# Kernel tuning notes

Measured on AMD Instinct MI355X. Metric: run time of the kernel, lower is better.

Reference implementation:

```python
import jax, jax.numpy as jnp
import numpy as np

BATCH, T, IN, HID = 64, 2048, 128, 256

def setup_inputs() -> dict:
    key = jax.random.key(0)
    ks = jax.random.split(key, 6)
    s = 0.05
    return {
        "x": jax.random.normal(ks[0], (BATCH, T, IN), dtype=jnp.float32),
        "w_ih0": jax.random.normal(ks[1], (IN, 4 * HID), dtype=jnp.float32) * s,
        "w_hh0": jax.random.normal(ks[2], (HID, 4 * HID), dtype=jnp.float32) * s,
        "b0": jnp.zeros((4 * HID,), dtype=jnp.float32),
        "w_ih1": jax.random.normal(ks[3], (HID, 4 * HID), dtype=jnp.float32) * s,
        "w_hh1": jax.random.normal(ks[4], (HID, 4 * HID), dtype=jnp.float32) * s,
        "b1": jnp.zeros((4 * HID,), dtype=jnp.float32),
    }

def _run_layer(xs, h0, c0, w_ih, w_hh, b):
    # xs: [T, B, D]. Original code iterates input_[T-1-t], i.e. reversed time.
    def step(carry, xt):
        h, c = carry
        gates = xt @ w_ih + h @ w_hh + b            # [B, 4H]
        f, i, o, g = jnp.split(gates, 4, axis=1)     # split order f,i,o,g as in source
        c1 = jax.nn.sigmoid(f) * c + jax.nn.sigmoid(i) * jnp.tanh(g)
        h1 = jax.nn.sigmoid(o) * jnp.tanh(c1)
        return (h1, c1), h1
    (hT, cT), ys = jax.lax.scan(step, (h0, c0), xs[::-1])
    return ys, hT, cT

def reference(x, w_ih0, w_hh0, b0, w_ih1, w_hh1, b1):
    xs = jnp.transpose(x, (1, 0, 2))                 # batch_first -> [T, B, IN]
    B = xs.shape[1]
    H = w_hh0.shape[0]
    h0 = jnp.zeros((B, H), dtype=xs.dtype)
    # Both layers start from the SAME zero hx (faithful to source).
    y0, hn0, cn0 = _run_layer(xs, h0, h0, w_ih0, w_hh0, b0)
    y1, hn1, cn1 = _run_layer(y0, h0, h0, w_ih1, w_hh1, b1)
    # Source never transposes output back: output is [T, B, H]
    return y1, (jnp.stack([hn0, hn1], 0), jnp.stack([cn0, cn1], 0))
```

## Files before the change

### kernel.cpp

```cpp
#include <hip/hip_runtime.h>
#include <cstdint>
#include <cstddef>

#define T_STEPS 2048
#define NBATCH  64
#define HID     256
#define NGATE   1024
#define NROWS   (T_STEPS*NBATCH)

#define KR   192
#define KRC  24
#define KLC  8
#define REC_LDS_BYTES (KLC*1024*16 + 4096 + 512)

typedef _Float16 f16x8 __attribute__((ext_vector_type(8)));
typedef _Float16 h2f   __attribute__((ext_vector_type(2)));
typedef float    f32x4 __attribute__((ext_vector_type(4)));

__device__ __forceinline__ unsigned short f2h_bits(float f) {
    _Float16 h = (_Float16)f;
    return __builtin_bit_cast(unsigned short, h);
}
__device__ __forceinline__ float h2f_scalar(unsigned short u) {
    return (float)__builtin_bit_cast(_Float16, u);
}
__device__ __forceinline__ h2f bch(unsigned int u) {
    return __builtin_bit_cast(h2f, u);
}

#define OFF_G    ((size_t)0)
#define OFF_Y0   ((size_t)268435456)
#define OFF_WT0  ((size_t)335544320)
#define OFF_WT1  ((size_t)336068608)
#define OFF_LW0  ((size_t)336592896)
#define OFF_LW1  ((size_t)336723968)
#define OFF_BS0  ((size_t)336855040)
#define OFF_BS1  ((size_t)337117184)
#define WS_NEED  ((size_t)337641472)

__global__ void convert_weights(const float* __restrict__ w_ih0, const float* __restrict__ w_hh0,
                                const float* __restrict__ w_ih1, const float* __restrict__ w_hh1,
                                unsigned short* __restrict__ WT0, unsigned short* __restrict__ WT1,
                                unsigned short* __restrict__ LW0, unsigned short* __restrict__ LW1,
                                unsigned short* __restrict__ BS0, unsigned short* __restrict__ BS1)
{
    int gid = blockIdx.x * blockDim.x + threadIdx.x;
    int gsz = gridDim.x * blockDim.x;
    for (int s = gid; s < 1024 * 256; s += gsz) {
        int j = s >> 8, k = s & 255;
        WT0[s] = f2h_bits(w_hh0[k * 1024 + j]);
        WT1[s] = f2h_bits(w_hh1[k * 1024 + j]);
    }
    for (int s = gid; s < KLC * 1024 * 8; s += gsz) {
        int i = s & 7, j = (s >> 3) & 1023, c = s >> 13;
        int k = KR + c * 8 + i;
        LW0[s] = f2h_bits(w_hh0[k * 1024 + j]);
        LW1[s] = f2h_bits(w_hh1[k * 1024 + j]);
    }
    for (int s = gid; s < 131072; s += gsz) {
        int i = s & 7, lane = (s >> 3) & 63, kb = (s >> 9) & 3, n16 = s >> 11;
        int k = kb * 32 + (lane >> 4) * 8 + i;
        int n = n16 * 16 + (lane & 15);
        BS0[s] = f2h_bits(w_ih0[k * 1024 + n]);
    }
    for (int s = gid; s < 262144; s += gsz) {
        int i = s & 7, lane = (s >> 3) & 63, kb = (s >> 9) & 7, n16 = s >> 12;
        int k = kb * 32 + (lane >> 4) * 8 + i;
        int n = n16 * 16 + (lane & 15);
        BS1[s] = f2h_bits(w_ih1[k * 1024 + n]);
    }
}

template <int KB, int LAYER>
__global__ __launch_bounds__(256) void gemm_in(const float* __restrict__ A32,
                                               const unsigned short* __restrict__ A16,
                                               const unsigned short* __restrict__ Bsw,
                                               const float* __restrict__ bias,
                                               unsigned short* __restrict__ Gout)
{
    const int lane = threadIdx.x & 63;
    const int wave = threadIdx.x >> 6;
    const int nblk = blockIdx.x & 15;
    const int rblk = blockIdx.x >> 4;
    const int r0 = rblk * 128 + wave * 32;
    const int quad = lane >> 4, ln = lane & 15;

    f32x4 acc[2][4];
#pragma unroll
    for (int q = 0; q < 4; q++) {
        float bv = bias[(nblk * 4 + q) * 16 + ln];
#pragma unroll
        for (int mt = 0; mt < 2; mt++) {
            acc[mt][q][0] = bv; acc[mt][q][1] = bv; acc[mt][q][2] = bv; acc[mt][q][3] = bv;
        }
    }
    const int ar0 = r0 + ln, ar1 = r0 + 16 + ln;
    size_t aoff0, aoff1;
    if (LAYER == 0) {
        aoff0 = ((size_t)(ar0 & 63) * 2048 + (size_t)(2047 - (ar0 >> 6))) * 128;
        aoff1 = ((size_t)(ar1 & 63) * 2048 + (size_t)(2047 - (ar1 >> 6))) * 128;
    } else {
        aoff0 = ((size_t)(2047 - (ar0 >> 6)) * 64 + (size_t)(ar0 & 63)) * 256;
        aoff1 = ((size_t)(2047 - (ar1 >> 6)) * 64 + (size_t)(ar1 & 63)) * 256;
    }
#pragma unroll
    for (int kb = 0; kb < KB; kb++) {
        const int k0 = kb * 32 + quad * 8;
        f16x8 a0, a1;
        if (LAYER == 0) {
            const float* p0 = A32 + aoff0 + k0;
            const float* p1 = A32 + aoff1 + k0;
            float4 fa = *(const float4*)(p0);
            float4 fb = *(const float4*)(p0 + 4);
            float4 fc = *(const float4*)(p1);
            float4 fd = *(const float4*)(p1 + 4);
            a0[0] = (_Float16)fa.x; a0[1] = (_Float16)fa.y; a0[2] = (_Float16)fa.z; a0[3] = (_Float16)fa.w;
            a0[4] = (_Float16)fb.x; a0[5] = (_Float16)fb.y; a0[6] = (_Float16)fb.z; a0[7] = (_Float16)fb.w;
            a1[0] = (_Float16)fc.x; a1[1] = (_Float16)fc.y; a1[2] = (_Float16)fc.z; a1[3] = (_Float16)fc.w;
            a1[4] = (_Float16)fd.x; a1[5] = (_Float16)fd.y; a1[6] = (_Float16)fd.z; a1[7] = (_Float16)fd.w;
        } else {
            a0 = *(const f16x8*)(A16 + aoff0 + k0);
            a1 = *(const f16x8*)(A16 + aoff1 + k0);
        }
#pragma unroll
        for (int q = 0; q < 4; q++) {
            f16x8 bq = *(const f16x8*)(Bsw + (((size_t)(nblk * 4 + q) * KB + kb) * 64 + lane) * 8);
            acc[0][q] = __builtin_amdgcn_mfma_f32_16x16x32_f16(a0, bq, acc[0][q], 0, 0, 0);
            acc[1][q] = __builtin_amdgcn_mfma_f32_16x16x32_f16(a1, bq, acc[1][q], 0, 0, 0);
        }
    }
#pragma unroll
    for (int mt = 0; mt < 2; mt++)
#pragma unroll
        for (int q = 0; q < 4; q++)
#pragma unroll
            for (int rg = 0; rg < 4; rg++) {
                int row = r0 + mt * 16 + quad * 4 + rg;
                int col = (nblk * 4 + q) * 16 + ln;
                Gout[(size_t)row * 1024 + col] = f2h_bits(acc[mt][q][rg]);
            }
}

template <int LAYER>
__global__ __launch_bounds__(512, 2) void lstm_rec(const unsigned short* __restrict__ G,
                                                   const unsigned short* __restrict__ WT,
                                                   const unsigned short* __restrict__ LW,
                                                   unsigned short* __restrict__ Y0,
                                                   float* __restrict__ Out)
{
    extern __shared__ char smem[];
    unsigned short* lds_w = (unsigned short*)smem;
    float* lds_g = (float*)(smem + (size_t)KLC * 1024 * 16);
    unsigned short* lds_h = (unsigned short*)(smem + (size_t)KLC * 1024 * 16 + 4096);

    const int b = blockIdx.x;
    const int tid = threadIdx.x;
    const int j0 = tid, j1 = tid + 512;

    uint4 wr0[KRC], wr1[KRC];
    {
        const uint4* p0 = (const uint4*)(WT + (size_t)j0 * 256);
        const uint4* p1 = (const uint4*)(WT + (size_t)j1 * 256);
#pragma unroll
        for (int i = 0; i < KRC; i++) { wr0[i] = p0[i]; wr1[i] = p1[i]; }
    }
    {
        const uint4* src = (const uint4*)LW;
        uint4* dst = (uint4*)lds_w;
        for (int i = tid; i < KLC * 1024; i += 512) dst[i] = src[i];
    }
    if (tid < 256) lds_h[tid] = 0;
    float c = 0.f;
    unsigned short gp0 = G[(size_t)b * 1024 + j0];
    unsigned short gp1 = G[(size_t)b * 1024 + j1];
    __syncthreads();

    for (int t = 0; t < T_STEPS; ++t) {
        float ga = h2f_scalar(gp0);
        float gb = h2f_scalar(gp1);
        {
            int tn = (t < T_STEPS - 1) ? t + 1 : t;
            const unsigned short* Gn = G + ((size_t)tn * 64 + b) * 1024;
            gp0 = Gn[j0]; gp1 = Gn[j1];
        }
        h2f a00 = {}, a01 = {}, a02 = {}, a03 = {};
        h2f a10 = {}, a11 = {}, a12 = {}, a13 = {};
        const uint4* hv = (const uint4*)lds_h;
#pragma unroll
        for (int ci = 0; ci < KRC; ++ci) {
            uint4 h4 = hv[ci];
            h2f h0 = bch(h4.x), h1 = bch(h4.y), h2v = bch(h4.z), h3 = bch(h4.w);
            uint4 w = wr0[ci];
            a00 += h0 * bch(w.x); a01 += h1 * bch(w.y); a02 += h2v * bch(w.z); a03 += h3 * bch(w.w);
            w = wr1[ci];
            a10 += h0 * bch(w.x); a11 += h1 * bch(w.y); a12 += h2v * bch(w.z); a13 += h3 * bch(w.w);
        }
        const uint4* wl = (const uint4*)lds_w;
#pragma unroll
        for (int ci = 0; ci < KLC; ++ci) {
            uint4 h4 = hv[KRC + ci];
            h2f h0 = bch(h4.x), h1 = bch(h4.y), h2v = bch(h4.z), h3 = bch(h4.w);
            uint4 w = wl[ci * 1024 + j0];
            a00 += h0 * bch(w.x); a01 += h1 * bch(w.y); a02 += h2v * bch(w.z); a03 += h3 * bch(w.w);
            w = wl[ci * 1024 + j1];
            a10 += h0 * bch(w.x); a11 += h1 * bch(w.y); a12 += h2v * bch(w.z); a13 += h3 * bch(w.w);
        }
        float gate0 = ga + ((float)a00.x + (float)a00.y) + ((float)a01.x + (float)a01.y)
                         + ((float)a02.x + (float)a02.y) + ((float)a03.x + (float)a03.y);
        float gate1 = gb + ((float)a10.x + (float)a10.y) + ((float)a11.x + (float)a11.y)
                         + ((float)a12.x + (float)a12.y) + ((float)a13.x + (float)a13.y);
        lds_g[j0] = gate0;
        lds_g[j1] = gate1;
        __syncthreads();
        if (tid < 256) {
            float f  = lds_g[tid];
            float ii = lds_g[tid + 256];
            float o  = lds_g[tid + 512];
            float g  = lds_g[tid + 768];
            float sf = 1.f / (1.f + __expf(-f));
            float si = 1.f / (1.f + __expf(-ii));
            float so = 1.f / (1.f + __expf(-o));
            float tg = 1.f - 2.f / (1.f + __expf(2.f * g));
            c = sf * c + si * tg;
            float tc = 1.f - 2.f / (1.f + __expf(2.f * c));
            float h = so * tc;
            lds_h[tid] = f2h_bits(h);
            if (LAYER == 0) {
                Y0[((size_t)t * 64 + b) * 256 + tid] = f2h_bits(h);
            } else {
                Out[((size_t)t * 64 + b) * 256 + tid] = h;
            }
            if (t == T_STEPS - 1) {
                Out[(size_t)33554432 + (size_t)LAYER * 16384 + (size_t)b * 256 + tid] = h;
                Out[(size_t)33554432 + 32768 + (size_t)LAYER * 16384 + (size_t)b * 256 + tid] = c;
            }
        }
        __syncthreads();
    }
}

extern "C" void kernel_launch(void* const* d_in, const int* in_sizes, int n_in,
                              void* d_out, int out_size, void* d_ws, size_t ws_size,
                              hipStream_t stream)
{
    const float* x     = (const float*)d_in[0];
    const float* w_ih0 = (const float*)d_in[1];
    const float* w_hh0 = (const float*)d_in[2];
    const float* b0    = (const float*)d_in[3];
    const float* w_ih1 = (const float*)d_in[4];
    const float* w_hh1 = (const float*)d_in[5];
    const float* b1    = (const float*)d_in[6];
    float* out = (float*)d_out;

    if (ws_size < WS_NEED) return;

    char* ws = (char*)d_ws;
    unsigned short* G   = (unsigned short*)(ws + OFF_G);
    unsigned short* Y0  = (unsigned short*)(ws + OFF_Y0);
    unsigned short* WT0 = (unsigned short*)(ws + OFF_WT0);
    unsigned short* WT1 = (unsigned short*)(ws + OFF_WT1);
    unsigned short* LW0 = (unsigned short*)(ws + OFF_LW0);
    unsigned short* LW1 = (unsigned short*)(ws + OFF_LW1);
    unsigned short* BS0 = (unsigned short*)(ws + OFF_BS0);
    unsigned short* BS1 = (unsigned short*)(ws + OFF_BS1);

    (void)hipFuncSetAttribute(reinterpret_cast<const void*>(&lstm_rec<0>),
                              hipFuncAttributeMaxDynamicSharedMemorySize, REC_LDS_BYTES);
    (void)hipFuncSetAttribute(reinterpret_cast<const void*>(&lstm_rec<1>),
                              hipFuncAttributeMaxDynamicSharedMemorySize, REC_LDS_BYTES);

    convert_weights<<<1024, 256, 0, stream>>>(w_ih0, w_hh0, w_ih1, w_hh1,
                                              WT0, WT1, LW0, LW1, BS0, BS1);
    gemm_in<4, 0><<<16384, 256, 0, stream>>>(x, nullptr, BS0, b0, G);
    lstm_rec<0><<<64, 512, REC_LDS_BYTES, stream>>>(G, WT0, LW0, Y0, out);
    gemm_in<8, 1><<<16384, 256, 0, stream>>>(nullptr, Y0, BS1, b1, G);
    lstm_rec<1><<<64, 512, REC_LDS_BYTES, stream>>>(G, WT1, LW1, Y0, out);
}
```

Before: 9.675 ms.

## Remap gate ownership to wave lanes, exchange gates via shuffles, double-buffer h

Reassigns gate columns so each wave's lane pair holds the f/i/o/g gates of the same hidden units, combining them with cross-half shuffles instead of an LDS gate buffer. This removes one of the two barriers per time step through ping-pong h buffers. The input-projection kernel writes gates in a swizzled layout so each thread reads its two gates as one packed 32-bit load. Packed half multiplies with half accumulators are replaced by fdot2 into float accumulators, and output stores are deferred by one step to leave the critical path.

New measurement: 8.210 ms. 15.1% less time.

```diff
diff --git a/kernel.cpp b/kernel.cpp
--- a/kernel.cpp
+++ b/kernel.cpp
@@ -6,12 +6,11 @@
 #define NBATCH  64
 #define HID     256
 #define NGATE   1024
-#define NROWS   (T_STEPS*NBATCH)
 
 #define KR   192
 #define KRC  24
 #define KLC  8
-#define REC_LDS_BYTES (KLC*1024*16 + 4096 + 512)
+#define REC_LDS_BYTES (KLC*1024*16 + 1024)
 
 typedef _Float16 f16x8 __attribute__((ext_vector_type(8)));
 typedef _Float16 h2f   __attribute__((ext_vector_type(2)));
@@ -24,8 +23,15 @@
 __device__ __forceinline__ float h2f_scalar(unsigned short u) {
     return (float)__builtin_bit_cast(_Float16, u);
 }
-__device__ __forceinline__ h2f bch(unsigned int u) {
-    return __builtin_bit_cast(h2f, u);
+
+__device__ __forceinline__ float fdot2u(unsigned int hh, unsigned int ww, float acc) {
+#if __has_builtin(__builtin_amdgcn_fdot2)
+    return __builtin_amdgcn_fdot2(__builtin_bit_cast(h2f, hh),
+                                  __builtin_bit_cast(h2f, ww), acc, false);
+#else
+    h2f a = __builtin_bit_cast(h2f, hh), b = __builtin_bit_cast(h2f, ww);
+    return acc + (float)a.x * (float)b.x + (float)a.y * (float)b.y;
+#endif
 }
 
 #define OFF_G    ((size_t)0)
@@ -137,7 +143,8 @@
             for (int rg = 0; rg < 4; rg++) {
                 int row = r0 + mt * 16 + quad * 4 + rg;
                 int col = (nblk * 4 + q) * 16 + ln;
-                Gout[(size_t)row * 1024 + col] = f2h_bits(acc[mt][q][rg]);
+                int swz = ((col & 255) << 2) | (col >> 8);
+                Gout[(size_t)row * 1024 + swz] = f2h_bits(acc[mt][q][rg]);
             }
 }
 
@@ -149,13 +156,17 @@
                                                    float* __restrict__ Out)
 {
     extern __shared__ char smem[];
-    unsigned short* lds_w = (unsigned short*)smem;
-    float* lds_g = (float*)(smem + (size_t)KLC * 1024 * 16);
-    unsigned short* lds_h = (unsigned short*)(smem + (size_t)KLC * 1024 * 16 + 4096);
+    unsigned short* lds_w  = (unsigned short*)smem;
+    unsigned short* lds_h0 = (unsigned short*)(smem + (size_t)KLC * 1024 * 16);
+    unsigned short* lds_h1 = lds_h0 + 256;
 
     const int b = blockIdx.x;
     const int tid = threadIdx.x;
-    const int j0 = tid, j1 = tid + 512;
+    const int wv = tid >> 6, l = tid & 63;
+    const int upper = l >> 5;
+    const int m = wv * 32 + (l & 31);
+    const int j0 = m + upper * 512;
+    const int j1 = j0 + 256;
 
     uint4 wr0[KRC], wr1[KRC];
     {
@@ -169,73 +180,69 @@
         uint4* dst = (uint4*)lds_w;
         for (int i = tid; i < KLC * 1024; i += 512) dst[i] = src[i];
     }
-    if (tid < 256) lds_h[tid] = 0;
-    float c = 0.f;
-    unsigned short gp0 = G[(size_t)b * 1024 + j0];
-    unsigned short gp1 = G[(size_t)b * 1024 + j1];
+    if (tid < 256) lds_h0[tid] = 0;
+    float c = 0.f, hprev = 0.f;
     __syncthreads();
 
+    const unsigned int* Gb = (const unsigned int*)G + (size_t)b * 512;
+
     for (int t = 0; t < T_STEPS; ++t) {
-        float ga = h2f_scalar(gp0);
-        float gb = h2f_scalar(gp1);
-        {
-            int tn = (t < T_STEPS - 1) ? t + 1 : t;
-            const unsigned short* Gn = G + ((size_t)tn * 64 + b) * 1024;
-            gp0 = Gn[j0]; gp1 = Gn[j1];
-        }
-        h2f a00 = {}, a01 = {}, a02 = {}, a03 = {};
-        h2f a10 = {}, a11 = {}, a12 = {}, a13 = {};
-        const uint4* hv = (const uint4*)lds_h;
+        unsigned int gpack = Gb[(size_t)t * 32768 + m * 2 + upper];
+        if (t && l < 32) {
+            if (LAYER == 0) Y0[((size_t)(t - 1) * 64 + b) * 256 + m] = f2h_bits(hprev);
+            else            Out[((size_t)(t - 1) * 64 + b) * 256 + m] = hprev;
+        }
+        const uint4* hv = (const uint4*)((t & 1) ? lds_h1 : lds_h0);
+        float a00 = 0, a01 = 0, a02 = 0, a03 = 0;
+        float a10 = 0, a11 = 0, a12 = 0, a13 = 0;
 #pragma unroll
         for (int ci = 0; ci < KRC; ++ci) {
             uint4 h4 = hv[ci];
-            h2f h0 = bch(h4.x), h1 = bch(h4.y), h2v = bch(h4.z), h3 = bch(h4.w);
             uint4 w = wr0[ci];
-            a00 += h0 * bch(w.x); a01 += h1 * bch(w.y); a02 += h2v * bch(w.z); a03 += h3 * bch(w.w);
+            a00 = fdot2u(h4.x, w.x, a00); a01 = fdot2u(h4.y, w.y, a01);
+            a02 = fdot2u(h4.z, w.z, a02); a03 = fdot2u(h4.w, w.w, a03);
             w = wr1[ci];
-            a10 += h0 * bch(w.x); a11 += h1 * bch(w.y); a12 += h2v * bch(w.z); a13 += h3 * bch(w.w);
-        }
-        const uint4* wl = (const uint4*)lds_w;
-#pragma unroll
-        for (int ci = 0; ci < KLC; ++ci) {
-            uint4 h4 = hv[KRC + ci];
-            h2f h0 = bch(h4.x), h1 = bch(h4.y), h2v = bch(h4.z), h3 = bch(h4.w);
-            uint4 w = wl[ci * 1024 + j0];
-            a00 += h0 * bch(w.x); a01 += h1 * bch(w.y); a02 += h2v * bch(w.z); a03 += h3 * bch(w.w);
-            w = wl[ci * 1024 + j1];
-            a10 += h0 * bch(w.x); a11 += h1 * bch(w.y); a12 += h2v * bch(w.z); a13 += h3 * bch(w.w);
-        }
-        float gate0 = ga + ((float)a00.x + (float)a00.y) + ((float)a01.x + (float)a01.y)
-                         + ((float)a02.x + (float)a02.y) + ((float)a03.x + (float)a03.y);
-        float gate1 = gb + ((float)a10.x + (float)a10.y) + ((float)a11.x + (float)a11.y)
-                         + ((float)a12.x + (float)a12.y) + ((float)a13.x + (float)a13.y);
-        lds_g[j0] = gate0;
-        lds_g[j1] = gate1;
+            a10 = fdot2u(h4.x, w.x, a10); a11 = fdot2u(h4.y, w.y, a11);
+            a12 = fdot2u(h4.z, w.z, a12); a13 = fdot2u(h4.w, w.w, a13);
+        }
+        {
+            const uint4* wl = (const uint4*)lds_w;
+#pragma unroll
+            for (int ci = 0; ci < KLC; ++ci) {
+                uint4 h4 = hv[KRC + ci];
+                uint4 w = wl[ci * 1024 + j0];
+                a00 = fdot2u(h4.x, w.x, a00); a01 = fdot2u(h4.y, w.y, a01);
+                a02 = fdot2u(h4.z, w.z, a02); a03 = fdot2u(h4.w, w.w, a03);
+                w = wl[ci * 1024 + j1];
+                a10 = fdot2u(h4.x, w.x, a10); a11 = fdot2u(h4.y, w.y, a11);
+                a12 = fdot2u(h4.z, w.z, a12); a13 = fdot2u(h4.w, w.w, a13);
+            }
+        }
+        float v0 = h2f_scalar((unsigned short)(gpack & 0xffff)) + ((a00 + a01) + (a02 + a03));
+        float v1 = h2f_scalar((unsigned short)(gpack >> 16))    + ((a10 + a11) + (a12 + a13));
+        float q0 = __shfl_xor(v0, 32, 64);
+        float q1 = __shfl_xor(v1, 32, 64);
+        float fg = upper ? q0 : v0;
+        float ig = upper ? q1 : v1;
+        float og = upper ? v0 : q0;
+        float gg = upper ? v1 : q1;
+        float sf = 1.f / (1.f + __expf(-fg));
+        float si = 1.f / (1.f + __expf(-ig));
+        float so = 1.f / (1.f + __expf(-og));
+        float tg = 1.f - 2.f / (1.f + __expf(2.f * gg));
+        c = sf * c + si * tg;
+        float tc = 1.f - 2.f / (1.f + __expf(2.f * c));
+        float h = so * tc;
+        hprev = h;
+        unsigned short* hn = (t & 1) ? lds_h0 : lds_h1;
+        if (l < 32) hn[m] = f2h_bits(h);
         __syncthreads();
-        if (tid < 256) {
-            float f  = lds_g[tid];
-            float ii = lds_g[tid + 256];
-            float o  = lds_g[tid + 512];
-            float g  = lds_g[tid + 768];
-            float sf = 1.f / (1.f + __expf(-f));
-            float si = 1.f / (1.f + __expf(-ii));
-            float so = 1.f / (1.f + __expf(-o));
-            float tg = 1.f - 2.f / (1.f + __expf(2.f * g));
-            c = sf * c + si * tg;
-            float tc = 1.f - 2.f / (1.f + __expf(2.f * c));
-            float h = so * tc;
-            lds_h[tid] = f2h_bits(h);
-            if (LAYER == 0) {
-                Y0[((size_t)t * 64 + b) * 256 + tid] = f2h_bits(h);
-            } else {
-                Out[((size_t)t * 64 + b) * 256 + tid] = h;
-            }
-            if (t == T_STEPS - 1) {
-                Out[(size_t)33554432 + (size_t)LAYER * 16384 + (size_t)b * 256 + tid] = h;
-                Out[(size_t)33554432 + 32768 + (size_t)LAYER * 16384 + (size_t)b * 256 + tid] = c;
-            }
-        }
-        __syncthreads();
+    }
+    if (l < 32) {
+        if (LAYER == 0) Y0[((size_t)(T_STEPS - 1) * 64 + b) * 256 + m] = f2h_bits(hprev);
+        else            Out[((size_t)(T_STEPS - 1) * 64 + b) * 256 + m] = hprev;
+        Out[(size_t)33554432 + (size_t)LAYER * 16384 + (size_t)b * 256 + m] = hprev;
+        Out[(size_t)33554432 + 32768 + (size_t)LAYER * 16384 + (size_t)b * 256 + m] = c;
     }
 }
 
```
